# Optimization experiments

Measured on AMD Instinct MI355X. Metric: run time of the kernel, lower is better.

Reference implementation:

```python
import jax, jax.numpy as jnp
import numpy as np

T = 16384
D_IN = 512
D_HID = 512
D_OUT = 512


def setup_inputs() -> dict:
    key = jax.random.key(0)
    ks = jax.random.split(key, 7)
    s_in = 1.0 / np.sqrt(D_IN)
    s_hid = 1.0 / np.sqrt(D_HID)
    xs = jax.random.normal(ks[0], (T, D_IN), dtype=jnp.float32)
    Wz = jax.random.uniform(ks[1], (D_HID, D_IN), jnp.float32, -s_in, s_in)
    bz = jax.random.uniform(ks[2], (D_HID,), jnp.float32, -s_in, s_in)
    Wh = jax.random.uniform(ks[3], (D_HID, D_IN), jnp.float32, -s_in, s_in)
    bh = jax.random.uniform(ks[4], (D_HID,), jnp.float32, -s_in, s_in)
    Wo = jax.random.uniform(ks[5], (D_OUT, D_HID), jnp.float32, -s_hid, s_hid)
    bo = jax.random.uniform(ks[6], (D_OUT,), jnp.float32, -s_hid, s_hid)
    return {"xs": xs, "Wz": Wz, "bz": bz, "Wh": Wh, "bh": bh, "Wo": Wo, "bo": bo}


def _combine(first, second):
    a0, b0 = first
    a1, b1 = second
    return (a0 * a1, a1 * b0 + b1)


def reference(xs, Wz, bz, Wh, bh, Wo, bo):
    # gates and candidate hidden states: [T, H]
    zs = jax.nn.sigmoid(xs @ Wz.T + bz)
    hs = xs @ Wh.T + bh
    # prepend identity element (a=1, b=0) for the h_0 = 0 initial state
    a = jnp.concatenate([jnp.ones((1, zs.shape[1]), zs.dtype), 1.0 - zs], axis=0)
    b = jnp.concatenate([jnp.zeros((1, zs.shape[1]), zs.dtype), zs * hs], axis=0)
    _, states = jax.lax.associative_scan(_combine, (a, b))  # [T+1, H]
    return states[1:] @ Wo.T + bo  # [T, D_OUT]
```

## Files before the change

### kernel.cpp

```cpp
#include <hip/hip_runtime.h>
#include <hip/hip_bf16.h>
#include <cstdint>
#include <cmath>

#define T_SEQ 16384
#define DMODEL 512
#define NCHUNK 512
#define LCHUNK 32
#define W_N    (DMODEL * DMODEL)
#define N4_W   (W_N / 4)
#define N4_W3  (3 * N4_W)
#define N4_X   (T_SEQ * DMODEL / 4)
#define N4_ALL (N4_W3 + N4_X)
#define BK     32
#define NT     (DMODEL / BK)

typedef __bf16 bf16x8 __attribute__((ext_vector_type(8)));
typedef float  f32x4  __attribute__((ext_vector_type(4)));

using bf16 = __hip_bfloat16;

__device__ __forceinline__ void load_lds16(const void* g, void* l) {
    __builtin_amdgcn_global_load_lds((const __attribute__((address_space(1))) void*)g,
                                     (__attribute__((address_space(3))) void*)l,
                                     16, 0, 0);
}

__device__ __forceinline__ unsigned short f2bf(float f) {
    union { float f; unsigned u; } v; v.f = f;
    const unsigned r = (v.u + 0x7FFFu + ((v.u >> 16) & 1u)) >> 16;
    return (unsigned short)r;
}
__device__ __forceinline__ float bf2f(unsigned short u) {
    union { unsigned u; float f; } v; v.u = ((unsigned)u) << 16;
    return v.f;
}

__device__ __forceinline__ void comb(float& A, float& B, float fA, float fB,
                                     float sA, float sB) {
    A = fA * sA;
    B = sA * fB + sB;
}

__global__ __launch_bounds__(256) void k_convert(
    const float* __restrict__ xs,
    const float* __restrict__ Wz, const float* __restrict__ Wh,
    const float* __restrict__ Wo,
    bf16* __restrict__ xs_c, bf16* __restrict__ Wz_c,
    bf16* __restrict__ Wh_c, bf16* __restrict__ Wo_c)
{
    const int i = blockIdx.x * 256 + threadIdx.x;
    if (i >= N4_ALL) return;
    const float* src; bf16* dst; int o;
    if (i < N4_W3) {
        const int w = i >> 16; o = i & 65535;
        src = (w == 0) ? Wz : (w == 1) ? Wh : Wo;
        dst = (w == 0) ? Wz_c : (w == 1) ? Wh_c : Wo_c;
    } else {
        o = i - N4_W3; src = xs; dst = xs_c;
    }
    const float4 v = ((const float4*)src)[o];
    ushort4 r;
    r.x = f2bf(v.x); r.y = f2bf(v.y); r.z = f2bf(v.z); r.w = f2bf(v.w);
    ((ushort4*)dst)[o] = r;
}

__global__ __launch_bounds__(256, 2) void gemm_zh(
    const bf16* __restrict__ xs_c, const bf16* __restrict__ Wz, const float* __restrict__ bz,
    const bf16* __restrict__ Wh, const float* __restrict__ bh,
    unsigned int* __restrict__ ab_ws,
    float* __restrict__ AaggT, float* __restrict__ BaggT)
{
    __shared__ __bf16 As[3][128 * BK];
    __shared__ __bf16 Zs[3][128 * BK];
    __shared__ __bf16 Hs[3][128 * BK];

    const int tid  = threadIdx.x;
    const int bm   = blockIdx.x;
    const int bn   = blockIdx.y;
    const int lane = tid & 63;
    const int wave = tid >> 6;
    const int wm   = wave >> 1;
    const int wn   = wave & 1;
    const int quad = lane >> 4;
    const int col  = lane & 15;

    f32x4 accz[4][4], acch[4][4];
    #pragma unroll
    for (int i = 0; i < 4; ++i)
        #pragma unroll
        for (int j = 0; j < 4; ++j) {
            accz[i][j] = (f32x4){0.f, 0.f, 0.f, 0.f};
            acch[i][j] = (f32x4){0.f, 0.f, 0.f, 0.f};
        }

    const int wrow = tid >> 2;
    const int wq   = (tid & 3) ^ ((tid >> 3) & 3);
    const bf16* ag = xs_c + (size_t)(bm * 128 + wrow) * DMODEL + wq * 8;
    const bf16* zg = Wz   + (size_t)(bn * 128 + wrow) * DMODEL + wq * 8;
    const bf16* hg = Wh   + (size_t)(bn * 128 + wrow) * DMODEL + wq * 8;

    const int fq = quad ^ ((col >> 1) & 3);
    int offA[4], offB[4];
    #pragma unroll
    for (int i = 0; i < 4; ++i) {
        offA[i] = (wm * 64 + i * 16 + col) * BK + fq * 8;
        offB[i] = (wn * 64 + i * 16 + col) * BK + fq * 8;
    }

    auto STAGE = [&](int t, int p) {
        const int k0 = t * BK;
        #pragma unroll
        for (int it = 0; it < 2; ++it) {
            const int chunk = it * 256 + tid;
            load_lds16(ag + (size_t)(it * 64) * DMODEL + k0, &As[p][chunk * 8]);
            load_lds16(zg + (size_t)(it * 64) * DMODEL + k0, &Zs[p][chunk * 8]);
            load_lds16(hg + (size_t)(it * 64) * DMODEL + k0, &Hs[p][chunk * 8]);
        }
    };
    auto COMPUTE = [&](int p) {
        bf16x8 af[4], zf[4], hf[4];
        #pragma unroll
        for (int i = 0; i < 4; ++i) {
            af[i] = *(const bf16x8*)&As[p][offA[i]];
            zf[i] = *(const bf16x8*)&Zs[p][offB[i]];
            hf[i] = *(const bf16x8*)&Hs[p][offB[i]];
        }
        #pragma unroll
        for (int i = 0; i < 4; ++i)
            #pragma unroll
            for (int j = 0; j < 4; ++j) {
                accz[i][j] = __builtin_amdgcn_mfma_f32_16x16x32_bf16(af[i], zf[j], accz[i][j], 0, 0, 0);
                acch[i][j] = __builtin_amdgcn_mfma_f32_16x16x32_bf16(af[i], hf[j], acch[i][j], 0, 0, 0);
            }
    };

    STAGE(0, 0); STAGE(1, 1);
    int pc = 0;
    for (int t = 0; t < NT - 1; ++t) {
        asm volatile("s_waitcnt vmcnt(6)" ::: "memory");
        __builtin_amdgcn_s_barrier();
        __builtin_amdgcn_sched_barrier(0);
        if (t + 2 < NT) {
            const int pn = (pc == 0) ? 2 : pc - 1;
            STAGE(t + 2, pn);
        }
        COMPUTE(pc);
        pc = (pc == 2) ? 0 : pc + 1;
    }
    asm volatile("s_waitcnt vmcnt(0)" ::: "memory");
    __builtin_amdgcn_s_barrier();
    __builtin_amdgcn_sched_barrier(0);
    COMPUTE(pc);

    const int c_lo = bm * 4 + wm * 2;
    #pragma unroll
    for (int j = 0; j < 4; ++j) {
        const int n = bn * 128 + wn * 64 + j * 16 + col;
        const float bzv = bz[n];
        const float bhv = bh[n];
        float cA[4], cB[4];
        #pragma unroll
        for (int i = 0; i < 4; ++i) {
            const int mbase = bm * 128 + wm * 64 + i * 16 + quad * 4;
            float A = 1.f, B = 0.f;
            #pragma unroll
            for (int r = 0; r < 4; ++r) {
                const float zpre = accz[i][j][r] + bzv;
                const float hpre = acch[i][j][r] + bhv;
                const float z = 1.f / (1.f + __expf(-zpre));
                const float a = 1.f - z;
                const float b = z * hpre;
                const size_t idx = (size_t)(mbase + r) * DMODEL + n;
                ab_ws[idx] = (unsigned)f2bf(a) | ((unsigned)f2bf(b) << 16);
                A = a * A;
                B = a * B + b;
            }
            cA[i] = A; cB[i] = B;
        }
        #pragma unroll
        for (int i = 0; i < 4; ++i) {
            float pA = __shfl_xor(cA[i], 16);
            float pB = __shfl_xor(cB[i], 16);
            const bool hi1 = quad & 1;
            comb(cA[i], cB[i], hi1 ? pA : cA[i], hi1 ? pB : cB[i],
                               hi1 ? cA[i] : pA, hi1 ? cB[i] : pB);
            pA = __shfl_xor(cA[i], 32);
            pB = __shfl_xor(cB[i], 32);
            const bool hi2 = quad >> 1;
            comb(cA[i], cB[i], hi2 ? pA : cA[i], hi2 ? pB : cB[i],
                               hi2 ? cA[i] : pA, hi2 ? cB[i] : pB);
        }
        float Alo, Blo, Ahi, Bhi;
        comb(Alo, Blo, cA[0], cB[0], cA[1], cB[1]);
        comb(Ahi, Bhi, cA[2], cB[2], cA[3], cB[3]);
        if (quad == 0) {
            AaggT[(size_t)n * NCHUNK + c_lo]     = Alo;
            BaggT[(size_t)n * NCHUNK + c_lo]     = Blo;
            AaggT[(size_t)n * NCHUNK + c_lo + 1] = Ahi;
            BaggT[(size_t)n * NCHUNK + c_lo + 1] = Bhi;
        }
    }
}

__global__ __launch_bounds__(512) void scan_p2(
    const float* __restrict__ AaggT, const float* __restrict__ BaggT,
    float* __restrict__ HpreT)
{
    const int h = blockIdx.x;
    const int c = threadIdx.x;
    __shared__ float sA[NCHUNK], sB[NCHUNK];

    float A = AaggT[(size_t)h * NCHUNK + c];
    float B = BaggT[(size_t)h * NCHUNK + c];
    sA[c] = A; sB[c] = B;
    __syncthreads();

    for (int off = 1; off < NCHUNK; off <<= 1) {
        float pA = 1.f, pB = 0.f;
        if (c >= off) { pA = sA[c - off]; pB = sB[c - off]; }
        __syncthreads();
        const float nB = A * pB + B;
        const float nA = A * pA;
        A = nA; B = nB;
        sA[c] = A; sB[c] = B;
        __syncthreads();
    }
    const float hp = (c == 0) ? 0.f : sB[c - 1];
    HpreT[(size_t)h * NCHUNK + c] = hp;
}

__global__ __launch_bounds__(256) void scan_p3(
    const unsigned int* __restrict__ ab_ws, const float* __restrict__ HpreT,
    unsigned short* __restrict__ states)
{
    const int tid = threadIdx.x;
    const int c   = blockIdx.x;
    const int ch  = blockIdx.y * 256 + tid;
    float H = HpreT[(size_t)ch * NCHUNK + c];
    const size_t base = (size_t)(c * LCHUNK) * DMODEL + ch;
    #pragma unroll 8
    for (int i = 0; i < LCHUNK; ++i) {
        const unsigned u = ab_ws[base + (size_t)i * DMODEL];
        const float a = bf2f((unsigned short)(u & 0xFFFFu));
        const float b = bf2f((unsigned short)(u >> 16));
        H = a * H + b;
        states[base + (size_t)i * DMODEL] = f2bf(H);
    }
}

__global__ __launch_bounds__(256, 3) void gemm_out(
    const bf16* __restrict__ states, const bf16* __restrict__ Wo, const float* __restrict__ bo,
    float* __restrict__ out)
{
    __shared__ __bf16 As[3][128 * BK];
    __shared__ __bf16 Bs[3][128 * BK];

    const int tid  = threadIdx.x;
    const int bm   = blockIdx.x;
    const int bn   = blockIdx.y;
    const int lane = tid & 63;
    const int wave = tid >> 6;
    const int wm   = wave >> 1;
    const int wn   = wave & 1;
    const int quad = lane >> 4;
    const int col  = lane & 15;

    f32x4 acc[4][4];
    #pragma unroll
    for (int i = 0; i < 4; ++i)
        #pragma unroll
        for (int j = 0; j < 4; ++j)
            acc[i][j] = (f32x4){0.f, 0.f, 0.f, 0.f};

    const int wrow = tid >> 2;
    const int wq   = (tid & 3) ^ ((tid >> 3) & 3);
    const bf16* ag = states + (size_t)(bm * 128 + wrow) * DMODEL + wq * 8;
    const bf16* bg = Wo     + (size_t)(bn * 128 + wrow) * DMODEL + wq * 8;

    const int fq = quad ^ ((col >> 1) & 3);
    int offA[4], offB[4];
    #pragma unroll
    for (int i = 0; i < 4; ++i) {
        offA[i] = (wm * 64 + i * 16 + col) * BK + fq * 8;
        offB[i] = (wn * 64 + i * 16 + col) * BK + fq * 8;
    }

    auto STAGE = [&](int t, int p) {
        const int k0 = t * BK;
        #pragma unroll
        for (int it = 0; it < 2; ++it) {
            const int chunk = it * 256 + tid;
            load_lds16(ag + (size_t)(it * 64) * DMODEL + k0, &As[p][chunk * 8]);
            load_lds16(bg + (size_t)(it * 64) * DMODEL + k0, &Bs[p][chunk * 8]);
        }
    };
    auto COMPUTE = [&](int p) {
        bf16x8 af[4], bf[4];
        #pragma unroll
        for (int i = 0; i < 4; ++i) {
            af[i] = *(const bf16x8*)&As[p][offA[i]];
            bf[i] = *(const bf16x8*)&Bs[p][offB[i]];
        }
        #pragma unroll
        for (int i = 0; i < 4; ++i)
            #pragma unroll
            for (int j = 0; j < 4; ++j)
                acc[i][j] = __builtin_amdgcn_mfma_f32_16x16x32_bf16(af[i], bf[j], acc[i][j], 0, 0, 0);
    };

    STAGE(0, 0); STAGE(1, 1);
    int pc = 0;
    for (int t = 0; t < NT - 1; ++t) {
        asm volatile("s_waitcnt vmcnt(4)" ::: "memory");
        __builtin_amdgcn_s_barrier();
        __builtin_amdgcn_sched_barrier(0);
        if (t + 2 < NT) {
            const int pn = (pc == 0) ? 2 : pc - 1;
            STAGE(t + 2, pn);
        }
        COMPUTE(pc);
        pc = (pc == 2) ? 0 : pc + 1;
    }
    asm volatile("s_waitcnt vmcnt(0)" ::: "memory");
    __builtin_amdgcn_s_barrier();
    __builtin_amdgcn_sched_barrier(0);
    COMPUTE(pc);

    #pragma unroll
    for (int j = 0; j < 4; ++j) {
        const int n = bn * 128 + wn * 64 + j * 16 + col;
        const float bov = bo[n];
        #pragma unroll
        for (int i = 0; i < 4; ++i) {
            const int mbase = bm * 128 + wm * 64 + i * 16 + quad * 4;
            #pragma unroll
            for (int r = 0; r < 4; ++r)
                out[(size_t)(mbase + r) * DMODEL + n] = acc[i][j][r] + bov;
        }
    }
}

extern "C" void kernel_launch(void* const* d_in, const int* in_sizes, int n_in,
                              void* d_out, int out_size, void* d_ws, size_t ws_size,
                              hipStream_t stream)
{
    const float* xs = (const float*)d_in[0];
    const float* Wz = (const float*)d_in[1];
    const float* bz = (const float*)d_in[2];
    const float* Wh = (const float*)d_in[3];
    const float* bh = (const float*)d_in[4];
    const float* Wo = (const float*)d_in[5];
    const float* bo = (const float*)d_in[6];
    float* out = (float*)d_out;

    char* w = (char*)d_ws;
    bf16*  Wz_c   = (bf16*) (w);
    bf16*  Wh_c   = (bf16*) (w + 524288ull);
    bf16*  Wo_c   = (bf16*) (w + 1048576ull);
    unsigned int*   ab_ws  = (unsigned int*)  (w + 1572864ull);
    unsigned short* states = (unsigned short*)(w + 35127296ull);
    float* AaggT  = (float*)(w + 51904512ull);
    float* BaggT  = (float*)(w + 52953088ull);
    float* HpreT  = (float*)(w + 54001664ull);
    bf16*  xs_c   = (bf16*) states;

    k_convert<<<(N4_ALL + 255) / 256, 256, 0, stream>>>(xs, Wz, Wh, Wo, xs_c, Wz_c, Wh_c, Wo_c);
    gemm_zh<<<dim3(128, 4), 256, 0, stream>>>(xs_c, Wz_c, bz, Wh_c, bh, ab_ws, AaggT, BaggT);
    scan_p2<<<DMODEL, NCHUNK, 0, stream>>>(AaggT, BaggT, HpreT);
    scan_p3<<<dim3(NCHUNK, 2), 256, 0, stream>>>(ab_ws, HpreT, states);
    gemm_out<<<dim3(128, 4), 256, 0, stream>>>((const bf16*)states, Wo_c, bo, out);
}
```

Measured before the change: 151.8 us.

## Enlarge GEMM tiles to 256x128 with 512 threads and split-K double buffering

Both bf16 MFMA GEMMs now use 256x128 output tiles computed by 8 waves, halving the grid. The K loop is restructured from a triple-buffered 32-wide stage into double-buffered 64-wide tiles, each loaded and consumed in two 32-wide halves, so loads overlap compute at finer grain. The MFMA bursts are wrapped in s_setprio raises. The intent is more operand reuse per LDS load and fewer blocks. In exchange, the larger LDS footprint (about 128KB for gemm_zh) likely limits occupancy to one block per CU, and the grid of 256 blocks leaves little room for load balancing.

```diff
diff --git a/kernel.cpp b/kernel.cpp
--- a/kernel.cpp
+++ b/kernel.cpp
@@ -12,8 +12,7 @@
 #define N4_W3  (3 * N4_W)
 #define N4_X   (T_SEQ * DMODEL / 4)
 #define N4_ALL (N4_W3 + N4_X)
-#define BK     32
-#define NT     (DMODEL / BK)
+#define NTILE  8
 
 typedef __bf16 bf16x8 __attribute__((ext_vector_type(8)));
 typedef float  f32x4  __attribute__((ext_vector_type(4)));
@@ -65,15 +64,15 @@
     ((ushort4*)dst)[o] = r;
 }
 
-__global__ __launch_bounds__(256, 2) void gemm_zh(
+__global__ __launch_bounds__(512, 2) void gemm_zh(
     const bf16* __restrict__ xs_c, const bf16* __restrict__ Wz, const float* __restrict__ bz,
     const bf16* __restrict__ Wh, const float* __restrict__ bh,
     unsigned int* __restrict__ ab_ws,
     float* __restrict__ AaggT, float* __restrict__ BaggT)
 {
-    __shared__ __bf16 As[3][128 * BK];
-    __shared__ __bf16 Zs[3][128 * BK];
-    __shared__ __bf16 Hs[3][128 * BK];
+    __shared__ __bf16 As[2][2][256 * 32];
+    __shared__ __bf16 Zs[2][2][128 * 32];
+    __shared__ __bf16 Hs[2][2][128 * 32];
 
     const int tid  = threadIdx.x;
     const int bm   = blockIdx.x;
@@ -94,66 +93,98 @@
             acch[i][j] = (f32x4){0.f, 0.f, 0.f, 0.f};
         }
 
-    const int wrow = tid >> 2;
+    const int srow = tid >> 2;
     const int wq   = (tid & 3) ^ ((tid >> 3) & 3);
-    const bf16* ag = xs_c + (size_t)(bm * 128 + wrow) * DMODEL + wq * 8;
-    const bf16* zg = Wz   + (size_t)(bn * 128 + wrow) * DMODEL + wq * 8;
-    const bf16* hg = Wh   + (size_t)(bn * 128 + wrow) * DMODEL + wq * 8;
+    const bf16* ag = xs_c + (size_t)(bm * 256 + srow) * DMODEL + wq * 8;
+    const bf16* zg = Wz   + (size_t)(bn * 128 + srow) * DMODEL + wq * 8;
+    const bf16* hg = Wh   + (size_t)(bn * 128 + srow) * DMODEL + wq * 8;
 
     const int fq = quad ^ ((col >> 1) & 3);
     int offA[4], offB[4];
     #pragma unroll
     for (int i = 0; i < 4; ++i) {
-        offA[i] = (wm * 64 + i * 16 + col) * BK + fq * 8;
-        offB[i] = (wn * 64 + i * 16 + col) * BK + fq * 8;
-    }
-
-    auto STAGE = [&](int t, int p) {
-        const int k0 = t * BK;
-        #pragma unroll
-        for (int it = 0; it < 2; ++it) {
-            const int chunk = it * 256 + tid;
-            load_lds16(ag + (size_t)(it * 64) * DMODEL + k0, &As[p][chunk * 8]);
-            load_lds16(zg + (size_t)(it * 64) * DMODEL + k0, &Zs[p][chunk * 8]);
-            load_lds16(hg + (size_t)(it * 64) * DMODEL + k0, &Hs[p][chunk * 8]);
-        }
+        offA[i] = (wm * 64 + i * 16 + col) * 32 + fq * 8;
+        offB[i] = (wn * 64 + i * 16 + col) * 32 + fq * 8;
+    }
+
+    auto STAGE_HALF = [&](int t, int h) {
+        const int b  = t & 1;
+        const int ko = t * 64 + h * 32;
+        load_lds16(ag + ko,                          &As[b][h][tid * 8]);
+        load_lds16(ag + (size_t)128 * DMODEL + ko,   &As[b][h][(512 + tid) * 8]);
+        load_lds16(zg + ko,                          &Zs[b][h][tid * 8]);
+        load_lds16(hg + ko,                          &Hs[b][h][tid * 8]);
     };
-    auto COMPUTE = [&](int p) {
+
+    STAGE_HALF(0, 0); STAGE_HALF(0, 1);
+
+    #pragma unroll
+    for (int t = 0; t < NTILE; ++t) {
+        const int b = t & 1;
         bf16x8 af[4], zf[4], hf[4];
-        #pragma unroll
-        for (int i = 0; i < 4; ++i) {
-            af[i] = *(const bf16x8*)&As[p][offA[i]];
-            zf[i] = *(const bf16x8*)&Zs[p][offB[i]];
-            hf[i] = *(const bf16x8*)&Hs[p][offB[i]];
-        }
-        #pragma unroll
-        for (int i = 0; i < 4; ++i)
-            #pragma unroll
-            for (int j = 0; j < 4; ++j) {
-                accz[i][j] = __builtin_amdgcn_mfma_f32_16x16x32_bf16(af[i], zf[j], accz[i][j], 0, 0, 0);
-                acch[i][j] = __builtin_amdgcn_mfma_f32_16x16x32_bf16(af[i], hf[j], acch[i][j], 0, 0, 0);
-            }
-    };
-
-    STAGE(0, 0); STAGE(1, 1);
-    int pc = 0;
-    for (int t = 0; t < NT - 1; ++t) {
-        asm volatile("s_waitcnt vmcnt(6)" ::: "memory");
+
+        asm volatile("s_waitcnt vmcnt(4)" ::: "memory");
         __builtin_amdgcn_s_barrier();
         __builtin_amdgcn_sched_barrier(0);
-        if (t + 2 < NT) {
-            const int pn = (pc == 0) ? 2 : pc - 1;
-            STAGE(t + 2, pn);
-        }
-        COMPUTE(pc);
-        pc = (pc == 2) ? 0 : pc + 1;
-    }
-    asm volatile("s_waitcnt vmcnt(0)" ::: "memory");
-    __builtin_amdgcn_s_barrier();
-    __builtin_amdgcn_sched_barrier(0);
-    COMPUTE(pc);
-
-    const int c_lo = bm * 4 + wm * 2;
+        if (t + 1 < NTILE) STAGE_HALF(t + 1, 0);
+        #pragma unroll
+        for (int i = 0; i < 4; ++i) {
+            af[i] = *(const bf16x8*)&As[b][0][offA[i]];
+            zf[i] = *(const bf16x8*)&Zs[b][0][offB[i]];
+        }
+        __builtin_amdgcn_s_setprio(1);
+        #pragma unroll
+        for (int i = 0; i < 4; ++i)
+            #pragma unroll
+            for (int j = 0; j < 4; ++j)
+                accz[i][j] = __builtin_amdgcn_mfma_f32_16x16x32_bf16(af[i], zf[j], accz[i][j], 0, 0, 0);
+        __builtin_amdgcn_s_setprio(0);
+
+        #pragma unroll
+        for (int j = 0; j < 4; ++j)
+            hf[j] = *(const bf16x8*)&Hs[b][0][offB[j]];
+        __builtin_amdgcn_s_setprio(1);
+        #pragma unroll
+        for (int i = 0; i < 4; ++i)
+            #pragma unroll
+            for (int j = 0; j < 4; ++j)
+                acch[i][j] = __builtin_amdgcn_mfma_f32_16x16x32_bf16(af[i], hf[j], acch[i][j], 0, 0, 0);
+        __builtin_amdgcn_s_setprio(0);
+
+        if (t + 1 < NTILE) {
+            asm volatile("s_waitcnt vmcnt(4)" ::: "memory");
+        } else {
+            asm volatile("s_waitcnt vmcnt(0)" ::: "memory");
+        }
+        __builtin_amdgcn_s_barrier();
+        __builtin_amdgcn_sched_barrier(0);
+        if (t + 1 < NTILE) STAGE_HALF(t + 1, 1);
+        #pragma unroll
+        for (int i = 0; i < 4; ++i) {
+            af[i] = *(const bf16x8*)&As[b][1][offA[i]];
+            zf[i] = *(const bf16x8*)&Zs[b][1][offB[i]];
+        }
+        __builtin_amdgcn_s_setprio(1);
+        #pragma unroll
+        for (int i = 0; i < 4; ++i)
+            #pragma unroll
+            for (int j = 0; j < 4; ++j)
+                accz[i][j] = __builtin_amdgcn_mfma_f32_16x16x32_bf16(af[i], zf[j], accz[i][j], 0, 0, 0);
+        __builtin_amdgcn_s_setprio(0);
+
+        #pragma unroll
+        for (int j = 0; j < 4; ++j)
+            hf[j] = *(const bf16x8*)&Hs[b][1][offB[j]];
+        __builtin_amdgcn_s_setprio(1);
+        #pragma unroll
+        for (int i = 0; i < 4; ++i)
+            #pragma unroll
+            for (int j = 0; j < 4; ++j)
+                acch[i][j] = __builtin_amdgcn_mfma_f32_16x16x32_bf16(af[i], hf[j], acch[i][j], 0, 0, 0);
+        __builtin_amdgcn_s_setprio(0);
+    }
+
+    const int c_lo = bm * 8 + wm * 2;
     #pragma unroll
     for (int j = 0; j < 4; ++j) {
         const int n = bn * 128 + wn * 64 + j * 16 + col;
@@ -162,7 +193,7 @@
         float cA[4], cB[4];
         #pragma unroll
         for (int i = 0; i < 4; ++i) {
-            const int mbase = bm * 128 + wm * 64 + i * 16 + quad * 4;
+            const int mbase = bm * 256 + wm * 64 + i * 16 + quad * 4;
             float A = 1.f, B = 0.f;
             #pragma unroll
             for (int r = 0; r < 4; ++r) {
@@ -249,12 +280,12 @@
     }
 }
 
-__global__ __launch_bounds__(256, 3) void gemm_out(
+__global__ __launch_bounds__(512, 2) void gemm_out(
     const bf16* __restrict__ states, const bf16* __restrict__ Wo, const float* __restrict__ bo,
     float* __restrict__ out)
 {
-    __shared__ __bf16 As[3][128 * BK];
-    __shared__ __bf16 Bs[3][128 * BK];
+    __shared__ __bf16 As[2][2][256 * 32];
+    __shared__ __bf16 Bs[2][2][128 * 32];
 
     const int tid  = threadIdx.x;
     const int bm   = blockIdx.x;
@@ -273,59 +304,72 @@
         for (int j = 0; j < 4; ++j)
             acc[i][j] = (f32x4){0.f, 0.f, 0.f, 0.f};
 
-    const int wrow = tid >> 2;
+    const int srow = tid >> 2;
     const int wq   = (tid & 3) ^ ((tid >> 3) & 3);
-    const bf16* ag = states + (size_t)(bm * 128 + wrow) * DMODEL + wq * 8;
-    const bf16* bg = Wo     + (size_t)(bn * 128 + wrow) * DMODEL + wq * 8;
+    const bf16* ag = states + (size_t)(bm * 256 + srow) * DMODEL + wq * 8;
+    const bf16* bg = Wo     + (size_t)(bn * 128 + srow) * DMODEL + wq * 8;
 
     const int fq = quad ^ ((col >> 1) & 3);
     int offA[4], offB[4];
     #pragma unroll
     for (int i = 0; i < 4; ++i) {
-        offA[i] = (wm * 64 + i * 16 + col) * BK + fq * 8;
-        offB[i] = (wn * 64 + i * 16 + col) * BK + fq * 8;
-    }
-
-    auto STAGE = [&](int t, int p) {
-        const int k0 = t * BK;
-        #pragma unroll
-        for (int it = 0; it < 2; ++it) {
-            const int chunk = it * 256 + tid;
-            load_lds16(ag + (size_t)(it * 64) * DMODEL + k0, &As[p][chunk * 8]);
-            load_lds16(bg + (size_t)(it * 64) * DMODEL + k0, &Bs[p][chunk * 8]);
-        }
+        offA[i] = (wm * 64 + i * 16 + col) * 32 + fq * 8;
+        offB[i] = (wn * 64 + i * 16 + col) * 32 + fq * 8;
+    }
+
+    auto STAGE_HALF = [&](int t, int h) {
+        const int b  = t & 1;
+        const int ko = t * 64 + h * 32;
+        load_lds16(ag + ko,                        &As[b][h][tid * 8]);
+        load_lds16(ag + (size_t)128 * DMODEL + ko, &As[b][h][(512 + tid) * 8]);
+        load_lds16(bg + ko,                        &Bs[b][h][tid * 8]);
     };
-    auto COMPUTE = [&](int p) {
+
+    STAGE_HALF(0, 0); STAGE_HALF(0, 1);
+
+    #pragma unroll
+    for (int t = 0; t < NTILE; ++t) {
+        const int b = t & 1;
         bf16x8 af[4], bf[4];
-        #pragma unroll
-        for (int i = 0; i < 4; ++i) {
-            af[i] = *(const bf16x8*)&As[p][offA[i]];
-            bf[i] = *(const bf16x8*)&Bs[p][offB[i]];
-        }
-        #pragma unroll
-        for (int i = 0; i < 4; ++i)
-            #pragma unroll
-            for (int j = 0; j < 4; ++j)
-                acc[i][j] = __builtin_amdgcn_mfma_f32_16x16x32_bf16(af[i], bf[j], acc[i][j], 0, 0, 0);
-    };
-
-    STAGE(0, 0); STAGE(1, 1);
-    int pc = 0;
-    for (int t = 0; t < NT - 1; ++t) {
-        asm volatile("s_waitcnt vmcnt(4)" ::: "memory");
+
+        asm volatile("s_waitcnt vmcnt(3)" ::: "memory");
         __builtin_amdgcn_s_barrier();
         __builtin_amdgcn_sched_barrier(0);
-        if (t + 2 < NT) {
-            const int pn = (pc == 0) ? 2 : pc - 1;
-            STAGE(t + 2, pn);
-        }
-        COMPUTE(pc);
-        pc = (pc == 2) ? 0 : pc + 1;
-    }
-    asm volatile("s_waitcnt vmcnt(0)" ::: "memory");
-    __builtin_amdgcn_s_barrier();
-    __builtin_amdgcn_sched_barrier(0);
-    COMPUTE(pc);
+        if (t + 1 < NTILE) STAGE_HALF(t + 1, 0);
+        #pragma unroll
+        for (int i = 0; i < 4; ++i) {
+            af[i] = *(const bf16x8*)&As[b][0][offA[i]];
+            bf[i] = *(const bf16x8*)&Bs[b][0][offB[i]];
+        }
+        __builtin_amdgcn_s_setprio(1);
+        #pragma unroll
+        for (int i = 0; i < 4; ++i)
+            #pragma unroll
+            for (int j = 0; j < 4; ++j)
+                acc[i][j] = __builtin_amdgcn_mfma_f32_16x16x32_bf16(af[i], bf[j], acc[i][j], 0, 0, 0);
+        __builtin_amdgcn_s_setprio(0);
+
+        if (t + 1 < NTILE) {
+            asm volatile("s_waitcnt vmcnt(3)" ::: "memory");
+        } else {
+            asm volatile("s_waitcnt vmcnt(0)" ::: "memory");
+        }
+        __builtin_amdgcn_s_barrier();
+        __builtin_amdgcn_sched_barrier(0);
+        if (t + 1 < NTILE) STAGE_HALF(t + 1, 1);
+        #pragma unroll
+        for (int i = 0; i < 4; ++i) {
+            af[i] = *(const bf16x8*)&As[b][1][offA[i]];
+            bf[i] = *(const bf16x8*)&Bs[b][1][offB[i]];
+        }
+        __builtin_amdgcn_s_setprio(1);
+        #pragma unroll
+        for (int i = 0; i < 4; ++i)
+            #pragma unroll
+            for (int j = 0; j < 4; ++j)
+                acc[i][j] = __builtin_amdgcn_mfma_f32_16x16x32_bf16(af[i], bf[j], acc[i][j], 0, 0, 0);
+        __builtin_amdgcn_s_setprio(0);
+    }
 
     #pragma unroll
     for (int j = 0; j < 4; ++j) {
@@ -333,7 +377,7 @@
         const float bov = bo[n];
         #pragma unroll
         for (int i = 0; i < 4; ++i) {
-            const int mbase = bm * 128 + wm * 64 + i * 16 + quad * 4;
+            const int mbase = bm * 256 + wm * 64 + i * 16 + quad * 4;
             #pragma unroll
             for (int r = 0; r < 4; ++r)
                 out[(size_t)(mbase + r) * DMODEL + n] = acc[i][j][r] + bov;
@@ -366,8 +410,8 @@
     bf16*  xs_c   = (bf16*) states;
 
     k_convert<<<(N4_ALL + 255) / 256, 256, 0, stream>>>(xs, Wz, Wh, Wo, xs_c, Wz_c, Wh_c, Wo_c);
-    gemm_zh<<<dim3(128, 4), 256, 0, stream>>>(xs_c, Wz_c, bz, Wh_c, bh, ab_ws, AaggT, BaggT);
+    gemm_zh<<<dim3(64, 4), 512, 0, stream>>>(xs_c, Wz_c, bz, Wh_c, bh, ab_ws, AaggT, BaggT);
     scan_p2<<<DMODEL, NCHUNK, 0, stream>>>(AaggT, BaggT, HpreT);
     scan_p3<<<dim3(NCHUNK, 2), 256, 0, stream>>>(ab_ws, HpreT, states);
-    gemm_out<<<dim3(128, 4), 256, 0, stream>>>((const bf16*)states, Wo_c, bo, out);
-}
+    gemm_out<<<dim3(64, 4), 512, 0, stream>>>((const bf16*)states, Wo_c, bo, out);
+}
```

After: 150.2 us. Within noise of the previous version (-1.1%).

## Enlarge output GEMM tile to 256x128 with 8 waves and half-tile pipelining

Applied to the files above, without the earlier changes.

The output projection GEMM now uses 512-thread blocks computing 256x128 tiles, with K staged in 64-wide tiles split into two 32-wide halves that are double-buffered. Each half is prefetched while the other is computed, and MFMA sections raise wave priority. This targets better reuse of Wo per block and fewer blocks, at the cost of larger LDS usage (96 KB) and lower blocks-per-CU occupancy.

```diff
diff --git a/kernel.cpp b/kernel.cpp
--- a/kernel.cpp
+++ b/kernel.cpp
@@ -14,6 +14,7 @@
 #define N4_ALL (N4_W3 + N4_X)
 #define BK     32
 #define NT     (DMODEL / BK)
+#define NTILE  8
 
 typedef __bf16 bf16x8 __attribute__((ext_vector_type(8)));
 typedef float  f32x4  __attribute__((ext_vector_type(4)));
@@ -249,12 +250,12 @@
     }
 }
 
-__global__ __launch_bounds__(256, 3) void gemm_out(
+__global__ __launch_bounds__(512, 2) void gemm_out(
     const bf16* __restrict__ states, const bf16* __restrict__ Wo, const float* __restrict__ bo,
     float* __restrict__ out)
 {
-    __shared__ __bf16 As[3][128 * BK];
-    __shared__ __bf16 Bs[3][128 * BK];
+    __shared__ __bf16 As[2][2][256 * 32];
+    __shared__ __bf16 Bs[2][2][128 * 32];
 
     const int tid  = threadIdx.x;
     const int bm   = blockIdx.x;
@@ -273,59 +274,72 @@
         for (int j = 0; j < 4; ++j)
             acc[i][j] = (f32x4){0.f, 0.f, 0.f, 0.f};
 
-    const int wrow = tid >> 2;
+    const int srow = tid >> 2;
     const int wq   = (tid & 3) ^ ((tid >> 3) & 3);
-    const bf16* ag = states + (size_t)(bm * 128 + wrow) * DMODEL + wq * 8;
-    const bf16* bg = Wo     + (size_t)(bn * 128 + wrow) * DMODEL + wq * 8;
+    const bf16* ag = states + (size_t)(bm * 256 + srow) * DMODEL + wq * 8;
+    const bf16* bg = Wo     + (size_t)(bn * 128 + srow) * DMODEL + wq * 8;
 
     const int fq = quad ^ ((col >> 1) & 3);
     int offA[4], offB[4];
     #pragma unroll
     for (int i = 0; i < 4; ++i) {
-        offA[i] = (wm * 64 + i * 16 + col) * BK + fq * 8;
-        offB[i] = (wn * 64 + i * 16 + col) * BK + fq * 8;
-    }
-
-    auto STAGE = [&](int t, int p) {
-        const int k0 = t * BK;
-        #pragma unroll
-        for (int it = 0; it < 2; ++it) {
-            const int chunk = it * 256 + tid;
-            load_lds16(ag + (size_t)(it * 64) * DMODEL + k0, &As[p][chunk * 8]);
-            load_lds16(bg + (size_t)(it * 64) * DMODEL + k0, &Bs[p][chunk * 8]);
-        }
+        offA[i] = (wm * 64 + i * 16 + col) * 32 + fq * 8;
+        offB[i] = (wn * 64 + i * 16 + col) * 32 + fq * 8;
+    }
+
+    auto STAGE_HALF = [&](int t, int h) {
+        const int b  = t & 1;
+        const int ko = t * 64 + h * 32;
+        load_lds16(ag + ko,                        &As[b][h][tid * 8]);
+        load_lds16(ag + (size_t)128 * DMODEL + ko, &As[b][h][(512 + tid) * 8]);
+        load_lds16(bg + ko,                        &Bs[b][h][tid * 8]);
     };
-    auto COMPUTE = [&](int p) {
+
+    STAGE_HALF(0, 0); STAGE_HALF(0, 1);
+
+    #pragma unroll
+    for (int t = 0; t < NTILE; ++t) {
+        const int b = t & 1;
         bf16x8 af[4], bf[4];
-        #pragma unroll
-        for (int i = 0; i < 4; ++i) {
-            af[i] = *(const bf16x8*)&As[p][offA[i]];
-            bf[i] = *(const bf16x8*)&Bs[p][offB[i]];
-        }
+
+        asm volatile("s_waitcnt vmcnt(3)" ::: "memory");
+        __builtin_amdgcn_s_barrier();
+        __builtin_amdgcn_sched_barrier(0);
+        if (t + 1 < NTILE) STAGE_HALF(t + 1, 0);
+        #pragma unroll
+        for (int i = 0; i < 4; ++i) {
+            af[i] = *(const bf16x8*)&As[b][0][offA[i]];
+            bf[i] = *(const bf16x8*)&Bs[b][0][offB[i]];
+        }
+        __builtin_amdgcn_s_setprio(1);
         #pragma unroll
         for (int i = 0; i < 4; ++i)
             #pragma unroll
             for (int j = 0; j < 4; ++j)
                 acc[i][j] = __builtin_amdgcn_mfma_f32_16x16x32_bf16(af[i], bf[j], acc[i][j], 0, 0, 0);
-    };
-
-    STAGE(0, 0); STAGE(1, 1);
-    int pc = 0;
-    for (int t = 0; t < NT - 1; ++t) {
-        asm volatile("s_waitcnt vmcnt(4)" ::: "memory");
+        __builtin_amdgcn_s_setprio(0);
+
+        if (t + 1 < NTILE) {
+            asm volatile("s_waitcnt vmcnt(3)" ::: "memory");
+        } else {
+            asm volatile("s_waitcnt vmcnt(0)" ::: "memory");
+        }
         __builtin_amdgcn_s_barrier();
         __builtin_amdgcn_sched_barrier(0);
-        if (t + 2 < NT) {
-            const int pn = (pc == 0) ? 2 : pc - 1;
-            STAGE(t + 2, pn);
-        }
-        COMPUTE(pc);
-        pc = (pc == 2) ? 0 : pc + 1;
-    }
-    asm volatile("s_waitcnt vmcnt(0)" ::: "memory");
-    __builtin_amdgcn_s_barrier();
-    __builtin_amdgcn_sched_barrier(0);
-    COMPUTE(pc);
+        if (t + 1 < NTILE) STAGE_HALF(t + 1, 1);
+        #pragma unroll
+        for (int i = 0; i < 4; ++i) {
+            af[i] = *(const bf16x8*)&As[b][1][offA[i]];
+            bf[i] = *(const bf16x8*)&Bs[b][1][offB[i]];
+        }
+        __builtin_amdgcn_s_setprio(1);
+        #pragma unroll
+        for (int i = 0; i < 4; ++i)
+            #pragma unroll
+            for (int j = 0; j < 4; ++j)
+                acc[i][j] = __builtin_amdgcn_mfma_f32_16x16x32_bf16(af[i], bf[j], acc[i][j], 0, 0, 0);
+        __builtin_amdgcn_s_setprio(0);
+    }
 
     #pragma unroll
     for (int j = 0; j < 4; ++j) {
@@ -333,7 +347,7 @@
         const float bov = bo[n];
         #pragma unroll
         for (int i = 0; i < 4; ++i) {
-            const int mbase = bm * 128 + wm * 64 + i * 16 + quad * 4;
+            const int mbase = bm * 256 + wm * 64 + i * 16 + quad * 4;
             #pragma unroll
             for (int r = 0; r < 4; ++r)
                 out[(size_t)(mbase + r) * DMODEL + n] = acc[i][j][r] + bov;
@@ -369,5 +383,5 @@
     gemm_zh<<<dim3(128, 4), 256, 0, stream>>>(xs_c, Wz_c, bz, Wh_c, bh, ab_ws, AaggT, BaggT);
     scan_p2<<<DMODEL, NCHUNK, 0, stream>>>(AaggT, BaggT, HpreT);
     scan_p3<<<dim3(NCHUNK, 2), 256, 0, stream>>>(ab_ws, HpreT, states);
-    gemm_out<<<dim3(128, 4), 256, 0, stream>>>((const bf16*)states, Wo_c, bo, out);
-}
+    gemm_out<<<dim3(64, 4), 512, 0, stream>>>((const bf16*)states, Wo_c, bo, out);
+}
```

Measured after the change: 152.3 us. Within noise of the previous version (+0.4%).
